# Kernel optimization log

Measured on AMD Instinct MI355X. Metric: run time of the kernel, lower is better.

## Reference

```python
import jax, jax.numpy as jnp
import numpy as np

B, T, C = 16, 2048, 128
HEAD_SIZE = 128

def setup_inputs() -> dict:
    key = jax.random.key(0)
    k1, k2, k3, k4 = jax.random.split(key, 4)
    x = jax.random.normal(k1, (B, T, C), dtype=jnp.float32)
    # nn.Linear(N_EMBED, head_size, bias=False) weight shape: [head_size, N_EMBED]
    scale = (1.0 / np.sqrt(C)).astype(np.float32)
    Wq = jax.random.normal(k2, (HEAD_SIZE, C), dtype=jnp.float32) * scale
    Wk = jax.random.normal(k3, (HEAD_SIZE, C), dtype=jnp.float32) * scale
    Wv = jax.random.normal(k4, (HEAD_SIZE, C), dtype=jnp.float32) * scale
    return {"x": x, "Wq": Wq, "Wk": Wk, "Wv": Wv}

def reference(x, Wq, Wk, Wv):
    Bd, Td, Cd = x.shape
    q = jnp.einsum('btc,hc->bth', x, Wq)  # [B,T,H]
    k = jnp.einsum('btc,hc->bth', x, Wk)
    v = jnp.einsum('btc,hc->bth', x, Wv)
    # NOTE: original scales by C**-0.5 (embedding dim), not head_size**-0.5
    scores = jnp.einsum('bth,bsh->bts', q, k) * (Cd ** -0.5)  # [B,T,T]
    causal = jnp.tril(jnp.ones((Td, Td), dtype=bool))
    scores = jnp.where(causal, scores, -jnp.inf)
    attn = jax.nn.softmax(scores, axis=-1)
    out = jnp.einsum('bts,bsh->bth', attn, v)  # [B,T,H]
    return out
```

## Files before the change

kernel.cpp:

```cpp
#include <hip/hip_runtime.h>
#include <hip/hip_bf16.h>

#define BB 16
#define TT 2048
#define CC 128
#define HH 128
#define NQT128 16

typedef __bf16 bf16x8 __attribute__((ext_vector_type(8)));
typedef __bf16 bf16x4 __attribute__((ext_vector_type(4)));
typedef float  f32x4  __attribute__((ext_vector_type(4)));
typedef unsigned int u32x2 __attribute__((ext_vector_type(2)));

#define BTH       ((size_t)BB * TT * HH)
#define WBF_OFF   (3 * BTH)
#define PARTIAL_OFF_BYTES (3 * BTH * 2 + 3 * 128 * 128 * 2)
#define SLOT_BYTES 33280
#define SLOT_L_OFF 32768

static __device__ __forceinline__ bf16x8 load_cvt8(const float* p) {
    float4 a = *(const float4*)p;
    float4 b = *(const float4*)(p + 4);
    bf16x8 r;
    r[0] = (__bf16)a.x; r[1] = (__bf16)a.y; r[2] = (__bf16)a.z; r[3] = (__bf16)a.w;
    r[4] = (__bf16)b.x; r[5] = (__bf16)b.y; r[6] = (__bf16)b.z; r[7] = (__bf16)b.w;
    return r;
}

__global__ __launch_bounds__(256) void wcvt_kernel(
    const float* __restrict__ Wq, const float* __restrict__ Wk,
    const float* __restrict__ Wv, __bf16* __restrict__ wbf)
{
    int idx = blockIdx.x * 256 + threadIdx.x;
    int which = idx >> 11;
    int rem = idx & 2047;
    int blk = rem >> 8;
    int r2  = rem & 255;
    int ks   = r2 >> 6;
    int lane = r2 & 63;
    int quad = lane >> 4, l16 = lane & 15;
    const float* src = (which == 0) ? Wq : (which == 1) ? Wk : Wv;
    float sc = (which == 0) ? (0.08838834764831845f * 1.4426950408889634f) : 1.0f;
    const float* p = src + (size_t)(blk * 16 + l16) * CC + ks * 32 + quad * 8;
    bf16x8 v;
    #pragma unroll
    for (int j = 0; j < 8; ++j) v[j] = (__bf16)(p[j] * sc);
    *(bf16x8*)(wbf + (size_t)which * 16384 + (((size_t)(blk * 4 + ks)) << 9) + lane * 8) = v;
}

#define TR_QK 132
#define TR_V  68

__global__ __launch_bounds__(256) void proj_kernel(
    const float* __restrict__ x, __bf16* __restrict__ ws)
{
    __shared__ float  xs[64 * 132];
    __shared__ __bf16 tr[128 * TR_V];

    const int lane = threadIdx.x & 63;
    const int wave = threadIdx.x >> 6;
    const int quad = lane >> 4;
    const int l16  = lane & 15;
    const int tid  = threadIdx.x;
    const int m0 = blockIdx.x * 64;
    const int b  = m0 / TT;
    const int t0 = m0 % TT;

    const __bf16* Wbf = ws + WBF_OFF;
    __bf16* Qs = ws;
    __bf16* Ks = ws + BTH;
    __bf16* Vs = ws + 2 * BTH;

    const float* xg = x + (size_t)m0 * CC;
    #pragma unroll
    for (int t = 0; t < 8; ++t) {
        int f = t * 256 + tid;
        int row = f >> 5, c4 = f & 31;
        float4 v = *(const float4*)(xg + (size_t)f * 4);
        *(float4*)(&xs[row * 132 + c4 * 4]) = v;
    }
    __syncthreads();

    bf16x8 xf[4];
    #pragma unroll
    for (int ks = 0; ks < 4; ++ks)
        xf[ks] = load_cvt8(&xs[(wave * 16 + l16) * 132 + ks * 32 + quad * 8]);

    #pragma unroll
    for (int which = 0; which < 2; ++which) {
        const __bf16* Wb = Wbf + (size_t)which * 16384;
        __bf16* dst = which ? Ks : Qs;
        #pragma unroll
        for (int nt = 0; nt < 8; ++nt) {
            f32x4 acc = {0.f, 0.f, 0.f, 0.f};
            #pragma unroll
            for (int ks = 0; ks < 4; ++ks) {
                bf16x8 wf = *(const bf16x8*)(Wb + (((size_t)(nt * 4 + ks)) << 9) + lane * 8);
                acc = __builtin_amdgcn_mfma_f32_16x16x32_bf16(xf[ks], wf, acc, 0, 0, 0);
            }
            #pragma unroll
            for (int r = 0; r < 4; ++r)
                tr[(wave * 16 + quad * 4 + r) * TR_QK + nt * 16 + l16] = (__bf16)acc[r];
        }
        asm volatile("s_waitcnt lgkmcnt(0)" ::: "memory");
        #pragma unroll
        for (int ks = 0; ks < 4; ++ks) {
            const __bf16* p = &tr[(wave * 16 + l16) * TR_QK + ks * 32 + quad * 8];
            uint2 lo = *(const uint2*)p;
            uint2 hi = *(const uint2*)(p + 4);
            uint4 v; v.x = lo.x; v.y = lo.y; v.z = hi.x; v.w = hi.y;
            __bf16* o = dst + (((size_t)(b * 128 + t0 / 16 + wave) * 4 + ks) << 9) + lane * 8;
            *(uint4*)o = v;
        }
        asm volatile("s_waitcnt lgkmcnt(0)" ::: "memory");
    }

    __syncthreads();
    const __bf16* Wv = Wbf + 2 * 16384;
    #pragma unroll
    for (int msub = 0; msub < 8; ++msub) {
        f32x4 acc = {0.f, 0.f, 0.f, 0.f};
        #pragma unroll
        for (int ks = 0; ks < 4; ++ks) {
            bf16x8 wf = *(const bf16x8*)(Wv + (((size_t)(msub * 4 + ks)) << 9) + lane * 8);
            acc = __builtin_amdgcn_mfma_f32_16x16x32_bf16(wf, xf[ks], acc, 0, 0, 0);
        }
        #pragma unroll
        for (int r = 0; r < 4; ++r)
            tr[(msub * 16 + quad * 4 + r) * TR_V + wave * 16 + l16] = (__bf16)acc[r];
    }
    __syncthreads();
    #pragma unroll
    for (int i = 0; i < 4; ++i) {
        int t32 = i >> 1;
        int h16 = wave * 2 + (i & 1);
        const __bf16* p = &tr[(h16 * 16 + l16) * TR_V + t32 * 32 + quad * 8];
        uint2 lo = *(const uint2*)p;
        uint2 hi = *(const uint2*)(p + 4);
        uint4 v; v.x = lo.x; v.y = lo.y; v.z = hi.x; v.w = hi.y;
        __bf16* o = Vs + (((size_t)(b * 64 + t0 / 32 + t32) * 8 + h16) << 9) + lane * 8;
        *(uint4*)o = v;
    }
}

__global__ __launch_bounds__(256) void attn_kernel(
    const __bf16* __restrict__ ws, char* __restrict__ po,
    float* __restrict__ outp, int G, int SPB, int direct)
{
    const int lane = threadIdx.x & 63;
    const int wave = threadIdx.x >> 6;
    const int quad = lane >> 4;
    const int l16  = lane & 15;
    const int lane8 = lane * 8;

    const int lin = blockIdx.x;
    const int b  = (lin & 7) * 2 + ((lin >> 3) & 1);
    const int s  = SPB - 1 - (lin >> 4);

    int acc = 0, qt = 0, seg = 0;
    for (int q = 0; q < NQT128; ++q) {
        int c = (2 * (q + 1) + G - 1) / G;
        if (s < acc + c) { qt = q; seg = s - acc; break; }
        acc += c;
    }
    const int kt0 = seg * G;
    int kt1 = 2 * (qt + 1);
    if (kt0 + G < kt1) kt1 = kt0 + G;
    const int segs_qt = (2 * (qt + 1) + G - 1) / G;
    const int dwrite = direct | (segs_qt == 1);

    const int tt0 = kt0 * 2, tt1 = kt1 * 2;
    const int qw = qt * 128 + wave * 32;
    int ttw = (qw + 63) >> 5;
    if (ttw > tt1) ttw = tt1;

    const __bf16* Qs = ws;
    const __bf16* Kb = ws + BTH     + (size_t)b * 262144;
    const __bf16* Vb = ws + 2 * BTH + (size_t)b * 262144;

    bf16x8 qf[2][4];
    #pragma unroll
    for (int m = 0; m < 2; ++m)
        #pragma unroll
        for (int ks = 0; ks < 4; ++ks)
            qf[m][ks] = *(const bf16x8*)(Qs + (((size_t)(b * 128 + qt * 8 + wave * 2 + m) * 4 + ks) << 9) + lane8);

    float l_r[2] = {0.f, 0.f};
    f32x4 o[2][8];
    #pragma unroll
    for (int m = 0; m < 2; ++m)
        #pragma unroll
        for (int h8 = 0; h8 < 8; ++h8) o[m][h8] = (f32x4){0.f, 0.f, 0.f, 0.f};

    for (int tt = tt0; tt < ttw; ++tt) {
        const __bf16* kt = Kb + (size_t)tt * 4096;
        const __bf16* vt = Vb + (size_t)tt * 4096;

        f32x4 s2[2][2];
        #pragma unroll
        for (int nsub = 0; nsub < 2; ++nsub) {
            bf16x8 kfr[4];
            #pragma unroll
            for (int ks = 0; ks < 4; ++ks)
                kfr[ks] = *(const bf16x8*)(kt + (nsub * 4 + ks) * 512 + lane8);
            #pragma unroll
            for (int m = 0; m < 2; ++m) {
                f32x4 a2 = {0.f, 0.f, 0.f, 0.f};
                #pragma unroll
                for (int ks = 0; ks < 4; ++ks)
                    a2 = __builtin_amdgcn_mfma_f32_16x16x32_bf16(kfr[ks], qf[m][ks], a2, 0, 0, 0);
                s2[m][nsub] = a2;
            }
        }

        const int k0 = tt * 32;
        unsigned int du[2][2][2];
        #pragma unroll
        for (int m = 0; m < 2; ++m) {
            const int qrow = qw + m * 16 + l16;
            if (k0 + 31 > qw + m * 16) {
                #pragma unroll
                for (int nsub = 0; nsub < 2; ++nsub) {
                    const int kb = k0 + nsub * 16 + quad * 4;
                    union { bf16x4 v; unsigned int u[2]; } cv;
                    #pragma unroll
                    for (int r = 0; r < 4; ++r) {
                        float sv = (kb + r > qrow) ? -3e38f : s2[m][nsub][r];
                        float p = __builtin_amdgcn_exp2f(sv);
                        l_r[m] += p;
                        cv.v[r] = (__bf16)p;
                    }
                    du[m][nsub][0] = cv.u[0];
                    du[m][nsub][1] = cv.u[1];
                }
            } else {
                #pragma unroll
                for (int nsub = 0; nsub < 2; ++nsub) {
                    union { bf16x4 v; unsigned int u[2]; } cv;
                    #pragma unroll
                    for (int r = 0; r < 4; ++r) {
                        float p = __builtin_amdgcn_exp2f(s2[m][nsub][r]);
                        l_r[m] += p;
                        cv.v[r] = (__bf16)p;
                    }
                    du[m][nsub][0] = cv.u[0];
                    du[m][nsub][1] = cv.u[1];
                }
            }
        }

        bf16x8 pf[2];
        #pragma unroll
        for (int m = 0; m < 2; ++m) {
            union { unsigned int u[4]; bf16x8 v; } cc;
            #pragma unroll
            for (int h = 0; h < 2; ++h) {
                u32x2 t1 = __builtin_amdgcn_permlane32_swap(
                    du[m][0][h], du[m][1][h], false, false);
                u32x2 t2 = __builtin_amdgcn_permlane16_swap(
                    t1[0], t1[1], false, false);
                cc.u[h]     = t2[0];
                cc.u[2 + h] = t2[1];
            }
            pf[m] = cc.v;
        }

        #pragma unroll
        for (int h8 = 0; h8 < 8; ++h8) {
            bf16x8 v0 = *(const bf16x8*)(vt + h8 * 512 + lane8);
            #pragma unroll
            for (int m = 0; m < 2; ++m)
                o[m][h8] = __builtin_amdgcn_mfma_f32_16x16x32_bf16(pf[m], v0, o[m][h8], 0, 0, 0);
        }
    }

    #pragma unroll
    for (int m = 0; m < 2; ++m) {
        l_r[m] += __shfl_xor(l_r[m], 16, 64);
        l_r[m] += __shfl_xor(l_r[m], 32, 64);
    }

    if (dwrite) {
        #pragma unroll
        for (int m = 0; m < 2; ++m) {
            float inv[4];
            #pragma unroll
            for (int r = 0; r < 4; ++r)
                inv[r] = 1.0f / __shfl(l_r[m], (lane & 48) | (quad * 4 + r), 64);
            #pragma unroll
            for (int h8 = 0; h8 < 8; ++h8)
                #pragma unroll
                for (int r = 0; r < 4; ++r)
                    outp[(size_t)(b * TT + qw + m * 16 + quad * 4 + r) * HH + h8 * 16 + l16] = o[m][h8][r] * inv[r];
        }
    } else {
        char* slot = po + (size_t)(b * SPB + s) * SLOT_BYTES;
        __bf16* slot_o = (__bf16*)slot;
        float*  slot_l = (float*)(slot + SLOT_L_OFF);
        #pragma unroll
        for (int m = 0; m < 2; ++m) {
            #pragma unroll
            for (int h8 = 0; h8 < 8; ++h8)
                #pragma unroll
                for (int r = 0; r < 4; ++r)
                    slot_o[(size_t)(wave * 32 + m * 16 + quad * 4 + r) * 128 + h8 * 16 + l16] = (__bf16)o[m][h8][r];
            if (quad == 0)
                slot_l[wave * 32 + m * 16 + l16] = l_r[m];
        }
    }
}

__global__ __launch_bounds__(256) void reduce_kernel(
    const char* __restrict__ po, float* __restrict__ outp, int G, int SPB)
{
    __shared__ float lsum[32];
    const int qt  = blockIdx.x >> 2;
    const int qtr = blockIdx.x & 3;
    const int b   = blockIdx.y;
    const int tid = threadIdx.x;

    const int segs = (2 * (qt + 1) + G - 1) / G;
    if (segs == 1) return;

    int acc = 0;
    for (int qq = 0; qq < qt; ++qq) acc += (2 * (qq + 1) + G - 1) / G;
    const char* base = po + (size_t)(b * SPB + acc) * SLOT_BYTES;
    const int r0 = qtr * 32;

    if (tid < 32) {
        float v = 0.f;
        for (int sg = 0; sg < segs; ++sg)
            v += ((const float*)(base + (size_t)sg * SLOT_BYTES + SLOT_L_OFF))[r0 + tid];
        lsum[tid] = v;
    }
    __syncthreads();

    const int rsub = tid >> 4;
    const int cg   = tid & 15;
    float a[2][8];
    #pragma unroll
    for (int p = 0; p < 2; ++p)
        #pragma unroll
        for (int j = 0; j < 8; ++j) a[p][j] = 0.f;

    for (int sg = 0; sg < segs; ++sg) {
        const char* sb = base + (size_t)sg * SLOT_BYTES;
        #pragma unroll
        for (int p = 0; p < 2; ++p) {
            int row = r0 + rsub + p * 16;
            union { uint4 u; __bf16 h[8]; } v;
            v.u = *(const uint4*)(sb + ((size_t)row * 128 + cg * 8) * 2);
            #pragma unroll
            for (int j = 0; j < 8; ++j) a[p][j] += (float)v.h[j];
        }
    }

    #pragma unroll
    for (int p = 0; p < 2; ++p) {
        int row = r0 + rsub + p * 16;
        float inv = 1.0f / lsum[rsub + p * 16];
        float* op = outp + (size_t)(b * TT + qt * 128 + row) * HH + cg * 8;
        float4 o0 = {a[p][0] * inv, a[p][1] * inv, a[p][2] * inv, a[p][3] * inv};
        float4 o1 = {a[p][4] * inv, a[p][5] * inv, a[p][6] * inv, a[p][7] * inv};
        *(float4*)op = o0;
        *(float4*)(op + 4) = o1;
    }
}

extern "C" void kernel_launch(void* const* d_in, const int* in_sizes, int n_in,
                              void* d_out, int out_size, void* d_ws, size_t ws_size,
                              hipStream_t stream)
{
    const float* x  = (const float*)d_in[0];
    const float* Wq = (const float*)d_in[1];
    const float* Wk = (const float*)d_in[2];
    const float* Wv = (const float*)d_in[3];
    __bf16* ws = (__bf16*)d_ws;
    float* out = (float*)d_out;
    char* po   = (char*)d_ws + PARTIAL_OFF_BYTES;

    int G = 0, SPB = 0, direct = 1;
    const int cand[5] = {4, 5, 6, 8, 16};
    for (int ci = 0; ci < 5; ++ci) {
        int g = cand[ci], spb = 0;
        for (int q = 0; q < NQT128; ++q) spb += (2 * (q + 1) + g - 1) / g;
        size_t need = PARTIAL_OFF_BYTES + (size_t)spb * BB * SLOT_BYTES;
        if (need <= ws_size) { G = g; SPB = spb; direct = 0; break; }
    }
    if (direct) { G = 2 * NQT128; SPB = NQT128; }

    wcvt_kernel<<<24, 256, 0, stream>>>(Wq, Wk, Wv, ws + WBF_OFF);
    proj_kernel<<<512, 256, 0, stream>>>(x, ws);
    attn_kernel<<<SPB * 16, 256, 0, stream>>>(ws, po, out, G, SPB, direct);
    if (!direct) {
        dim3 rgrid(NQT128 * 4, BB);
        reduce_kernel<<<rgrid, 256, 0, stream>>>(po, out, G, SPB);
    }
}
```

Baseline: 133.0 us.

## Stage K/V tiles in LDS with double-buffered async loads, drop split-K reduce

Rewrites the attention kernel so each block stages shared K/V tiles into double-buffered LDS using global_load_lds, and all four waves read them from LDS instead of each loading from global memory. The split-K partial/reduce path is removed. Load balance now comes from pairing query tiles qt and 15-qt across two passes per block, with the head dimension split into two halves across blocks. Each wave handles 16 query rows and 64 head columns, and MFMA sections get raised priority with s_setprio. Trade-offs: Q·K^T is recomputed for both head halves, and every tile step adds barriers and vmcnt waits.

```diff
diff --git a/kernel.cpp b/kernel.cpp
--- a/kernel.cpp
+++ b/kernel.cpp
@@ -14,9 +14,6 @@
 
 #define BTH       ((size_t)BB * TT * HH)
 #define WBF_OFF   (3 * BTH)
-#define PARTIAL_OFF_BYTES (3 * BTH * 2 + 3 * 128 * 128 * 2)
-#define SLOT_BYTES 33280
-#define SLOT_L_OFF 32768
 
 static __device__ __forceinline__ bf16x8 load_cvt8(const float* p) {
     float4 a = *(const float4*)p;
@@ -25,6 +22,12 @@
     r[0] = (__bf16)a.x; r[1] = (__bf16)a.y; r[2] = (__bf16)a.z; r[3] = (__bf16)a.w;
     r[4] = (__bf16)b.x; r[5] = (__bf16)b.y; r[6] = (__bf16)b.z; r[7] = (__bf16)b.w;
     return r;
+}
+
+static __device__ __forceinline__ void load_lds16(const void* g, void* l) {
+    __builtin_amdgcn_global_load_lds(
+        (const __attribute__((address_space(1))) unsigned int*)g,
+        (__attribute__((address_space(3))) unsigned int*)l, 16, 0, 0);
 }
 
 __global__ __launch_bounds__(256) void wcvt_kernel(
@@ -144,227 +147,165 @@
 }
 
 __global__ __launch_bounds__(256) void attn_kernel(
-    const __bf16* __restrict__ ws, char* __restrict__ po,
-    float* __restrict__ outp, int G, int SPB, int direct)
+    const __bf16* __restrict__ ws, float* __restrict__ outp)
 {
+    __shared__ char ldsBuf[2][24576];
+
     const int lane = threadIdx.x & 63;
     const int wave = threadIdx.x >> 6;
     const int quad = lane >> 4;
     const int l16  = lane & 15;
     const int lane8 = lane * 8;
+    const int lo16 = lane * 16;
 
     const int lin = blockIdx.x;
-    const int b  = (lin & 7) * 2 + ((lin >> 3) & 1);
-    const int s  = SPB - 1 - (lin >> 4);
-
-    int acc = 0, qt = 0, seg = 0;
-    for (int q = 0; q < NQT128; ++q) {
-        int c = (2 * (q + 1) + G - 1) / G;
-        if (s < acc + c) { qt = q; seg = s - acc; break; }
-        acc += c;
-    }
-    const int kt0 = seg * G;
-    int kt1 = 2 * (qt + 1);
-    if (kt0 + G < kt1) kt1 = kt0 + G;
-    const int segs_qt = (2 * (qt + 1) + G - 1) / G;
-    const int dwrite = direct | (segs_qt == 1);
-
-    const int tt0 = kt0 * 2, tt1 = kt1 * 2;
-    const int qw = qt * 128 + wave * 32;
-    int ttw = (qw + 63) >> 5;
-    if (ttw > tt1) ttw = tt1;
+    const int b   = (lin & 7) * 2 + ((lin >> 3) & 1);
+    const int rest = lin >> 4;
+    const int pid  = rest & 7;
+    const int hh0  = (rest >> 3) & 1;
+    const int mh   = 1 - (rest >> 4);
 
     const __bf16* Qs = ws;
-    const __bf16* Kb = ws + BTH     + (size_t)b * 262144;
-    const __bf16* Vb = ws + 2 * BTH + (size_t)b * 262144;
-
-    bf16x8 qf[2][4];
-    #pragma unroll
-    for (int m = 0; m < 2; ++m)
+    const __bf16* Ks = ws + BTH;
+    const __bf16* Vs = ws + 2 * BTH;
+
+    const char* kg = (const char*)Ks + (size_t)b * 524288 + wave * 4096 + lo16;
+    const char* vg = (const char*)Vs + (size_t)b * 524288 + hh0 * 4096 + wave * 1024 + lo16;
+
+    #define STAGE64(J, BUF)                                                     \
+        do {                                                                    \
+            char* dK_ = ldsBuf[BUF] + wave * 4096;                              \
+            char* dV_ = ldsBuf[BUF] + 16384 + wave * 1024;                      \
+            const char* sk_ = kg + (size_t)(J) * 16384;                         \
+            _Pragma("unroll")                                                   \
+            for (int c_ = 0; c_ < 4; ++c_)                                      \
+                load_lds16(sk_ + c_ * 1024, dK_ + c_ * 1024);                   \
+            _Pragma("unroll")                                                   \
+            for (int h_ = 0; h_ < 2; ++h_)                                      \
+                load_lds16(vg + (size_t)(2 * (J) + h_) * 8192, dV_ + h_ * 4096);\
+        } while (0)
+
+    #pragma unroll 1
+    for (int pass = 0; pass < 2; ++pass) {
+        const int qt = pass ? (15 - pid) : pid;
+        const int qw = qt * 128 + mh * 64 + wave * 16;
+        const int ttw = (qw >> 5) + 1;
+        const int nj  = 2 * qt + mh + 1;
+
+        bf16x8 qf[4];
         #pragma unroll
         for (int ks = 0; ks < 4; ++ks)
-            qf[m][ks] = *(const bf16x8*)(Qs + (((size_t)(b * 128 + qt * 8 + wave * 2 + m) * 4 + ks) << 9) + lane8);
-
-    float l_r[2] = {0.f, 0.f};
-    f32x4 o[2][8];
-    #pragma unroll
-    for (int m = 0; m < 2; ++m)
-        #pragma unroll
-        for (int h8 = 0; h8 < 8; ++h8) o[m][h8] = (f32x4){0.f, 0.f, 0.f, 0.f};
-
-    for (int tt = tt0; tt < ttw; ++tt) {
-        const __bf16* kt = Kb + (size_t)tt * 4096;
-        const __bf16* vt = Vb + (size_t)tt * 4096;
-
-        f32x4 s2[2][2];
-        #pragma unroll
-        for (int nsub = 0; nsub < 2; ++nsub) {
-            bf16x8 kfr[4];
+            qf[ks] = *(const bf16x8*)(Qs + (((size_t)(b * 128 + qt * 8 + mh * 4 + wave) * 4 + ks) << 9) + lane8);
+
+        float l_r = 0.f;
+        f32x4 o[4];
+        #pragma unroll
+        for (int h8 = 0; h8 < 4; ++h8) o[h8] = (f32x4){0.f, 0.f, 0.f, 0.f};
+
+        STAGE64(0, 0);
+        asm volatile("s_waitcnt vmcnt(0)" ::: "memory");
+        __builtin_amdgcn_s_barrier();
+
+        for (int j = 0; j < nj; ++j) {
+            const int cur = j & 1;
+            if (j + 1 < nj) STAGE64(j + 1, cur ^ 1);
+
             #pragma unroll
-            for (int ks = 0; ks < 4; ++ks)
-                kfr[ks] = *(const bf16x8*)(kt + (nsub * 4 + ks) * 512 + lane8);
-            #pragma unroll
-            for (int m = 0; m < 2; ++m) {
-                f32x4 a2 = {0.f, 0.f, 0.f, 0.f};
-                #pragma unroll
-                for (int ks = 0; ks < 4; ++ks)
-                    a2 = __builtin_amdgcn_mfma_f32_16x16x32_bf16(kfr[ks], qf[m][ks], a2, 0, 0, 0);
-                s2[m][nsub] = a2;
-            }
-        }
-
-        const int k0 = tt * 32;
-        unsigned int du[2][2][2];
-        #pragma unroll
-        for (int m = 0; m < 2; ++m) {
-            const int qrow = qw + m * 16 + l16;
-            if (k0 + 31 > qw + m * 16) {
+            for (int half = 0; half < 2; ++half) {
+                const int tt = 2 * j + half;
+                if (tt >= ttw) continue;
+                const char* lk = ldsBuf[cur] + half * 8192;
+                const char* lv = ldsBuf[cur] + 16384 + half * 4096;
+
+                f32x4 s2[2];
                 #pragma unroll
                 for (int nsub = 0; nsub < 2; ++nsub) {
-                    const int kb = k0 + nsub * 16 + quad * 4;
-                    union { bf16x4 v; unsigned int u[2]; } cv;
-                    #pragma unroll
-                    for (int r = 0; r < 4; ++r) {
-                        float sv = (kb + r > qrow) ? -3e38f : s2[m][nsub][r];
-                        float p = __builtin_amdgcn_exp2f(sv);
-                        l_r[m] += p;
-                        cv.v[r] = (__bf16)p;
+                    bf16x8 kfr[4];
+                    #pragma unroll
+                    for (int ks = 0; ks < 4; ++ks)
+                        kfr[ks] = *(const bf16x8*)(lk + ((nsub * 4 + ks) << 10) + lo16);
+                    f32x4 a2 = {0.f, 0.f, 0.f, 0.f};
+                    __builtin_amdgcn_s_setprio(1);
+                    #pragma unroll
+                    for (int ks = 0; ks < 4; ++ks)
+                        a2 = __builtin_amdgcn_mfma_f32_16x16x32_bf16(kfr[ks], qf[ks], a2, 0, 0, 0);
+                    __builtin_amdgcn_s_setprio(0);
+                    s2[nsub] = a2;
+                }
+
+                const int k0 = tt * 32;
+                unsigned int du[2][2];
+                const int qrow = qw + l16;
+                if (k0 + 31 > qw) {
+                    #pragma unroll
+                    for (int nsub = 0; nsub < 2; ++nsub) {
+                        const int kb = k0 + nsub * 16 + quad * 4;
+                        union { bf16x4 v; unsigned int u[2]; } cv;
+                        #pragma unroll
+                        for (int r = 0; r < 4; ++r) {
+                            float sv = (kb + r > qrow) ? -3e38f : s2[nsub][r];
+                            float p = __builtin_amdgcn_exp2f(sv);
+                            l_r += p;
+                            cv.v[r] = (__bf16)p;
+                        }
+                        du[nsub][0] = cv.u[0];
+                        du[nsub][1] = cv.u[1];
                     }
-                    du[m][nsub][0] = cv.u[0];
-                    du[m][nsub][1] = cv.u[1];
+                } else {
+                    #pragma unroll
+                    for (int nsub = 0; nsub < 2; ++nsub) {
+                        union { bf16x4 v; unsigned int u[2]; } cv;
+                        #pragma unroll
+                        for (int r = 0; r < 4; ++r) {
+                            float p = __builtin_amdgcn_exp2f(s2[nsub][r]);
+                            l_r += p;
+                            cv.v[r] = (__bf16)p;
+                        }
+                        du[nsub][0] = cv.u[0];
+                        du[nsub][1] = cv.u[1];
+                    }
                 }
-            } else {
+
+                bf16x8 pf;
+                {
+                    union { unsigned int u[4]; bf16x8 v; } cc;
+                    #pragma unroll
+                    for (int h = 0; h < 2; ++h) {
+                        u32x2 t1 = __builtin_amdgcn_permlane32_swap(
+                            du[0][h], du[1][h], false, false);
+                        u32x2 t2 = __builtin_amdgcn_permlane16_swap(
+                            t1[0], t1[1], false, false);
+                        cc.u[h]     = t2[0];
+                        cc.u[2 + h] = t2[1];
+                    }
+                    pf = cc.v;
+                }
+
+                __builtin_amdgcn_s_setprio(1);
                 #pragma unroll
-                for (int nsub = 0; nsub < 2; ++nsub) {
-                    union { bf16x4 v; unsigned int u[2]; } cv;
-                    #pragma unroll
-                    for (int r = 0; r < 4; ++r) {
-                        float p = __builtin_amdgcn_exp2f(s2[m][nsub][r]);
-                        l_r[m] += p;
-                        cv.v[r] = (__bf16)p;
-                    }
-                    du[m][nsub][0] = cv.u[0];
-                    du[m][nsub][1] = cv.u[1];
+                for (int h8 = 0; h8 < 4; ++h8) {
+                    bf16x8 v0 = *(const bf16x8*)(lv + (h8 << 10) + lo16);
+                    o[h8] = __builtin_amdgcn_mfma_f32_16x16x32_bf16(pf, v0, o[h8], 0, 0, 0);
                 }
+                __builtin_amdgcn_s_setprio(0);
             }
+            asm volatile("s_waitcnt vmcnt(0)" ::: "memory");
+            __builtin_amdgcn_s_barrier();
         }
 
-        bf16x8 pf[2];
-        #pragma unroll
-        for (int m = 0; m < 2; ++m) {
-            union { unsigned int u[4]; bf16x8 v; } cc;
-            #pragma unroll
-            for (int h = 0; h < 2; ++h) {
-                u32x2 t1 = __builtin_amdgcn_permlane32_swap(
-                    du[m][0][h], du[m][1][h], false, false);
-                u32x2 t2 = __builtin_amdgcn_permlane16_swap(
-                    t1[0], t1[1], false, false);
-                cc.u[h]     = t2[0];
-                cc.u[2 + h] = t2[1];
-            }
-            pf[m] = cc.v;
-        }
-
-        #pragma unroll
-        for (int h8 = 0; h8 < 8; ++h8) {
-            bf16x8 v0 = *(const bf16x8*)(vt + h8 * 512 + lane8);
-            #pragma unroll
-            for (int m = 0; m < 2; ++m)
-                o[m][h8] = __builtin_amdgcn_mfma_f32_16x16x32_bf16(pf[m], v0, o[m][h8], 0, 0, 0);
-        }
-    }
-
-    #pragma unroll
-    for (int m = 0; m < 2; ++m) {
-        l_r[m] += __shfl_xor(l_r[m], 16, 64);
-        l_r[m] += __shfl_xor(l_r[m], 32, 64);
-    }
-
-    if (dwrite) {
-        #pragma unroll
-        for (int m = 0; m < 2; ++m) {
-            float inv[4];
+        l_r += __shfl_xor(l_r, 16, 64);
+        l_r += __shfl_xor(l_r, 32, 64);
+        float inv[4];
+        #pragma unroll
+        for (int r = 0; r < 4; ++r)
+            inv[r] = 1.0f / __shfl(l_r, (lane & 48) | (quad * 4 + r), 64);
+        #pragma unroll
+        for (int h8 = 0; h8 < 4; ++h8)
             #pragma unroll
             for (int r = 0; r < 4; ++r)
-                inv[r] = 1.0f / __shfl(l_r[m], (lane & 48) | (quad * 4 + r), 64);
-            #pragma unroll
-            for (int h8 = 0; h8 < 8; ++h8)
-                #pragma unroll
-                for (int r = 0; r < 4; ++r)
-                    outp[(size_t)(b * TT + qw + m * 16 + quad * 4 + r) * HH + h8 * 16 + l16] = o[m][h8][r] * inv[r];
-        }
-    } else {
-        char* slot = po + (size_t)(b * SPB + s) * SLOT_BYTES;
-        __bf16* slot_o = (__bf16*)slot;
-        float*  slot_l = (float*)(slot + SLOT_L_OFF);
-        #pragma unroll
-        for (int m = 0; m < 2; ++m) {
-            #pragma unroll
-            for (int h8 = 0; h8 < 8; ++h8)
-                #pragma unroll
-                for (int r = 0; r < 4; ++r)
-                    slot_o[(size_t)(wave * 32 + m * 16 + quad * 4 + r) * 128 + h8 * 16 + l16] = (__bf16)o[m][h8][r];
-            if (quad == 0)
-                slot_l[wave * 32 + m * 16 + l16] = l_r[m];
-        }
-    }
-}
-
-__global__ __launch_bounds__(256) void reduce_kernel(
-    const char* __restrict__ po, float* __restrict__ outp, int G, int SPB)
-{
-    __shared__ float lsum[32];
-    const int qt  = blockIdx.x >> 2;
-    const int qtr = blockIdx.x & 3;
-    const int b   = blockIdx.y;
-    const int tid = threadIdx.x;
-
-    const int segs = (2 * (qt + 1) + G - 1) / G;
-    if (segs == 1) return;
-
-    int acc = 0;
-    for (int qq = 0; qq < qt; ++qq) acc += (2 * (qq + 1) + G - 1) / G;
-    const char* base = po + (size_t)(b * SPB + acc) * SLOT_BYTES;
-    const int r0 = qtr * 32;
-
-    if (tid < 32) {
-        float v = 0.f;
-        for (int sg = 0; sg < segs; ++sg)
-            v += ((const float*)(base + (size_t)sg * SLOT_BYTES + SLOT_L_OFF))[r0 + tid];
-        lsum[tid] = v;
-    }
-    __syncthreads();
-
-    const int rsub = tid >> 4;
-    const int cg   = tid & 15;
-    float a[2][8];
-    #pragma unroll
-    for (int p = 0; p < 2; ++p)
-        #pragma unroll
-        for (int j = 0; j < 8; ++j) a[p][j] = 0.f;
-
-    for (int sg = 0; sg < segs; ++sg) {
-        const char* sb = base + (size_t)sg * SLOT_BYTES;
-        #pragma unroll
-        for (int p = 0; p < 2; ++p) {
-            int row = r0 + rsub + p * 16;
-            union { uint4 u; __bf16 h[8]; } v;
-            v.u = *(const uint4*)(sb + ((size_t)row * 128 + cg * 8) * 2);
-            #pragma unroll
-            for (int j = 0; j < 8; ++j) a[p][j] += (float)v.h[j];
-        }
-    }
-
-    #pragma unroll
-    for (int p = 0; p < 2; ++p) {
-        int row = r0 + rsub + p * 16;
-        float inv = 1.0f / lsum[rsub + p * 16];
-        float* op = outp + (size_t)(b * TT + qt * 128 + row) * HH + cg * 8;
-        float4 o0 = {a[p][0] * inv, a[p][1] * inv, a[p][2] * inv, a[p][3] * inv};
-        float4 o1 = {a[p][4] * inv, a[p][5] * inv, a[p][6] * inv, a[p][7] * inv};
-        *(float4*)op = o0;
-        *(float4*)(op + 4) = o1;
-    }
+                outp[(size_t)(b * TT + qw + quad * 4 + r) * HH + hh0 * 64 + h8 * 16 + l16] = o[h8][r] * inv[r];
+    }
+    #undef STAGE64
 }
 
 extern "C" void kernel_launch(void* const* d_in, const int* in_sizes, int n_in,
@@ -377,23 +318,8 @@
     const float* Wv = (const float*)d_in[3];
     __bf16* ws = (__bf16*)d_ws;
     float* out = (float*)d_out;
-    char* po   = (char*)d_ws + PARTIAL_OFF_BYTES;
-
-    int G = 0, SPB = 0, direct = 1;
-    const int cand[5] = {4, 5, 6, 8, 16};
-    for (int ci = 0; ci < 5; ++ci) {
-        int g = cand[ci], spb = 0;
-        for (int q = 0; q < NQT128; ++q) spb += (2 * (q + 1) + g - 1) / g;
-        size_t need = PARTIAL_OFF_BYTES + (size_t)spb * BB * SLOT_BYTES;
-        if (need <= ws_size) { G = g; SPB = spb; direct = 0; break; }
-    }
-    if (direct) { G = 2 * NQT128; SPB = NQT128; }
 
     wcvt_kernel<<<24, 256, 0, stream>>>(Wq, Wk, Wv, ws + WBF_OFF);
     proj_kernel<<<512, 256, 0, stream>>>(x, ws);
-    attn_kernel<<<SPB * 16, 256, 0, stream>>>(ws, po, out, G, SPB, direct);
-    if (!direct) {
-        dim3 rgrid(NQT128 * 4, BB);
-        reduce_kernel<<<rgrid, 256, 0, stream>>>(po, out, G, SPB);
-    }
-}
+    attn_kernel<<<512, 256, 0, stream>>>(ws, out);
+}
```

Result: faster. 127.1 us (-4.5%).
